# Kernel optimization log

Measured on AMD Instinct MI355X. Metric: run time of the kernel, lower is better.

## Reference

```python
import jax, jax.numpy as jnp
import numpy as np

BATCH = 8192
IN_F = 1024
OUT_F = 1024
GRID_SIZE = 5
SPLINE_ORDER = 3
GRID_LO, GRID_HI = -1.0, 1.0


def setup_inputs() -> dict:
    key = jax.random.key(0)
    k1, k2, k3, k4 = jax.random.split(key, 4)
    x = jax.random.normal(k1, (BATCH, IN_F), dtype=jnp.float32)
    # grid buffer: extended knot vector, same for every input feature
    h = (GRID_HI - GRID_LO) / GRID_SIZE
    knots = jnp.linspace(GRID_LO - SPLINE_ORDER * h, GRID_HI + SPLINE_ORDER * h,
                         GRID_SIZE + 2 * SPLINE_ORDER + 1, dtype=jnp.float32)
    grid = jnp.tile(knots[None, :], (IN_F, 1))  # [in, 12]
    fan_in_scale = 1.0 / np.sqrt(IN_F)
    base_weight = jax.random.normal(k2, (OUT_F, IN_F), dtype=jnp.float32) * fan_in_scale
    spline_weight = jax.random.normal(k3, (IN_F, GRID_SIZE + SPLINE_ORDER, OUT_F), dtype=jnp.float32) * 0.1
    spline_scaler = jax.random.normal(k4, (IN_F, OUT_F), dtype=jnp.float32) * fan_in_scale
    return {"x": x, "grid": grid, "base_weight": base_weight,
            "spline_weight": spline_weight, "spline_scaler": spline_scaler}


def b_splines(x, grid):
    """Cox-de Boor recursion. x: [B, in], grid: [in, G+2k+1] -> [B, in, G+k]."""
    xe = x[:, :, None]  # [B, in, 1]
    bases = ((xe >= grid[:, :-1]) & (xe < grid[:, 1:])).astype(x.dtype)  # [B, in, G+2k]
    for k in range(1, SPLINE_ORDER + 1):
        left = (xe - grid[:, :-(k + 1)]) / (grid[:, k:-1] - grid[:, :-(k + 1)])
        right = (grid[:, k + 1:] - xe) / (grid[:, k + 1:] - grid[:, 1:-k])
        bases = left * bases[:, :, :-1] + right * bases[:, :, 1:]
    return bases  # [B, in, G+k]


def reference(x, grid, base_weight, spline_weight, spline_scaler):
    # base branch: SiLU(x) @ W_base^T
    base_out = jax.nn.silu(x) @ base_weight.T  # [B, out]
    # spline branch
    basis = b_splines(x, grid)  # [B, in, G+k]
    scaled_w = spline_weight * spline_scaler[:, None, :]  # [in, G+k, out]
    spline_out = jnp.einsum('bik,iko->bo', basis, scaled_w)  # [B, out]
    return base_out + spline_out
```

## Files before the change

### kernel.cpp

```cpp
#include <hip/hip_runtime.h>
#include <cstdint>
#include <cstddef>

#define BATCH 8192
#define IN_F 1024
#define OUT_F 1024
#define NSPL 9
#define KDIM (IN_F * NSPL)

typedef __bf16 bf16x8 __attribute__((ext_vector_type(8)));
typedef float f32x4 __attribute__((ext_vector_type(4)));

__device__ __forceinline__ void g2l16(const void* g, void* l) {
  __builtin_amdgcn_global_load_lds(
      (__attribute__((address_space(1))) void*)(g),
      (__attribute__((address_space(3))) void*)(l),
      16, 0, 0);
}

__global__ void build_w(const float* __restrict__ bw, const float* __restrict__ sw,
                        const float* __restrict__ sc, __bf16* __restrict__ Wt) {
  __shared__ float s_sw[16 * 8 * 64];
  __shared__ float s_sc[16 * 64];
  __shared__ float s_bw[64 * 16];
  const int tid = threadIdx.x;
  const int o0 = (blockIdx.x & 15) * 64;
  const int i0 = (blockIdx.x >> 4) * 16;

#pragma unroll
  for (int it = 0; it < 32; ++it) {
    const int t = it * 256 + tid;
    const int i = t >> 9, r = (t >> 6) & 7, oo = t & 63;
    s_sw[t] = sw[((size_t)(i0 + i) * 8 + r) * OUT_F + o0 + oo];
  }
#pragma unroll
  for (int it = 0; it < 4; ++it) {
    const int t = it * 256 + tid;
    const int i = t >> 6, oo = t & 63;
    s_sc[t] = sc[(size_t)(i0 + i) * OUT_F + o0 + oo];
  }
#pragma unroll
  for (int it = 0; it < 4; ++it) {
    const int t = it * 256 + tid;
    const int oo = t >> 4, ii = t & 15;
    s_bw[t] = bw[(size_t)(o0 + oo) * IN_F + i0 + ii];
  }
  __syncthreads();

  const int oo = tid >> 2;
  const int isub = (tid & 3) * 4;
#pragma unroll
  for (int is = 0; is < 4; ++is) {
    const int i = isub + is;
    __bf16* dst = Wt + (size_t)(o0 + oo) * KDIM + (size_t)(i0 + i) * NSPL;
    dst[0] = (__bf16)s_bw[oo * 16 + i];
    const float scal = s_sc[i * 64 + oo];
#pragma unroll
    for (int r = 0; r < 8; ++r)
      dst[1 + r] = (__bf16)(s_sw[i * 512 + r * 64 + oo] * scal);
  }
}

__global__ void build_a(const float* __restrict__ x, __bf16* __restrict__ A) {
  __shared__ __align__(16) __bf16 rowbuf[KDIM];
  const int b = blockIdx.x;
  const int tid = threadIdx.x;
#pragma unroll
  for (int c = 0; c < IN_F / 256; ++c) {
    const int i = c * 256 + tid;
    const float v = x[(size_t)b * IN_F + i];
    float w[NSPL];
#pragma unroll
    for (int r = 0; r < NSPL; ++r) w[r] = 0.f;
    w[0] = v / (1.f + __expf(-v));
    const float p = (v + 2.2f) * 2.5f;
    const int cell = (int)floorf(p);
    if (cell >= 0 && cell <= 10 && v < 2.2f) {
      const float t = p - (float)cell;
      const float t2 = t * t, t3 = t2 * t;
      const float omt = 1.f - t;
      const float b0 = (1.f / 6.f) * omt * omt * omt;
      const float b1 = (1.f / 6.f) * (3.f * t3 - 6.f * t2 + 4.f);
      const float b2 = (1.f / 6.f) * (-3.f * t3 + 3.f * t2 + 3.f * t + 1.f);
      const float b3 = (1.f / 6.f) * t3;
      const int j0 = cell - 3;
      if (j0 + 0 >= 0 && j0 + 0 <= 7) w[1 + j0 + 0] = b0;
      if (j0 + 1 >= 0 && j0 + 1 <= 7) w[1 + j0 + 1] = b1;
      if (j0 + 2 >= 0 && j0 + 2 <= 7) w[1 + j0 + 2] = b2;
      if (j0 + 3 >= 0 && j0 + 3 <= 7) w[1 + j0 + 3] = b3;
    }
    __bf16* d = rowbuf + (size_t)i * NSPL;
#pragma unroll
    for (int r = 0; r < NSPL; ++r) d[r] = (__bf16)w[r];
  }
  __syncthreads();
  const uint4* src = (const uint4*)rowbuf;
  uint4* dst = (uint4*)(A + (size_t)b * KDIM);
  for (int t = tid; t < KDIM * 2 / 16; t += 256)
    dst[t] = src[t];
}

__global__ __launch_bounds__(256) void gemm_bt(const __bf16* __restrict__ A,
                                               const __bf16* __restrict__ W,
                                               float* __restrict__ out) {
  __shared__ __align__(16) __bf16 As[2 * 128 * 32];
  __shared__ __align__(16) __bf16 Bs[2 * 128 * 32];

  const int tid = threadIdx.x;
  const int wv = tid >> 6;
  const int lane = tid & 63;
  const int mb = blockIdx.x & 63;
  const int nb = blockIdx.x >> 6;
  const int m0 = mb * 128;
  const int n0 = nb * 128;
  const int wr = wv & 1;
  const int wc = wv >> 1;

  const int srow = lane >> 2;
  const int scol = (lane & 3) * 8;
  const __bf16* gA = A + (size_t)(m0 + wv * 32 + srow) * KDIM + scol;
  const __bf16* gB = W + (size_t)(n0 + wv * 32 + srow) * KDIM + scol;
  __bf16* lA = As + wv * 1024;
  __bf16* lB = Bs + wv * 1024;

  const int mrow = lane & 15;
  const int quad = lane >> 4;
  int aoff[4], boff[4];
#pragma unroll
  for (int mt = 0; mt < 4; ++mt) aoff[mt] = (wr * 64 + mt * 16 + mrow) * 32 + quad * 8;
#pragma unroll
  for (int nt = 0; nt < 4; ++nt) boff[nt] = (wc * 64 + nt * 16 + mrow) * 32 + quad * 8;

  f32x4 acc[4][4];
  const f32x4 zero = {0.f, 0.f, 0.f, 0.f};
#pragma unroll
  for (int mt = 0; mt < 4; ++mt)
#pragma unroll
    for (int nt = 0; nt < 4; ++nt) acc[mt][nt] = zero;

  for (int k0 = 0; k0 < KDIM; k0 += 64) {
    __syncthreads();
    g2l16(gA + k0, lA);
    g2l16(gA + k0 + (size_t)16 * KDIM, lA + 512);
    g2l16(gB + k0, lB);
    g2l16(gB + k0 + (size_t)16 * KDIM, lB + 512);
    g2l16(gA + k0 + 32, lA + 4096);
    g2l16(gA + k0 + 32 + (size_t)16 * KDIM, lA + 4096 + 512);
    g2l16(gB + k0 + 32, lB + 4096);
    g2l16(gB + k0 + 32 + (size_t)16 * KDIM, lB + 4096 + 512);
    __syncthreads();

    bf16x8 af[2][4], bfr[2][4];
#pragma unroll
    for (int h = 0; h < 2; ++h) {
#pragma unroll
      for (int mt = 0; mt < 4; ++mt) af[h][mt] = *(const bf16x8*)(As + h * 4096 + aoff[mt]);
#pragma unroll
      for (int nt = 0; nt < 4; ++nt) bfr[h][nt] = *(const bf16x8*)(Bs + h * 4096 + boff[nt]);
    }
#pragma unroll
    for (int h = 0; h < 2; ++h)
#pragma unroll
      for (int mt = 0; mt < 4; ++mt)
#pragma unroll
        for (int nt = 0; nt < 4; ++nt)
          acc[mt][nt] = __builtin_amdgcn_mfma_f32_16x16x32_bf16(af[h][mt], bfr[h][nt],
                                                                acc[mt][nt], 0, 0, 0);
  }

#pragma unroll
  for (int mt = 0; mt < 4; ++mt) {
#pragma unroll
    for (int nt = 0; nt < 4; ++nt) {
      const int col = n0 + wc * 64 + nt * 16 + mrow;
      const int rbase = m0 + wr * 64 + mt * 16 + quad * 4;
#pragma unroll
      for (int r = 0; r < 4; ++r)
        out[(size_t)(rbase + r) * OUT_F + col] = acc[mt][nt][r];
    }
  }
}

extern "C" void kernel_launch(void* const* d_in, const int* in_sizes, int n_in,
                              void* d_out, int out_size, void* d_ws, size_t ws_size,
                              hipStream_t stream) {
  const float* x  = (const float*)d_in[0];
  const float* bw = (const float*)d_in[2];
  const float* sw = (const float*)d_in[3];
  const float* sc = (const float*)d_in[4];
  float* out = (float*)d_out;

  __bf16* Wt = (__bf16*)d_ws;
  __bf16* Ab = (__bf16*)((char*)d_ws +
                         (size_t)OUT_F * KDIM * sizeof(__bf16));

  build_w<<<1024, 256, 0, stream>>>(bw, sw, sc, Wt);
  build_a<<<BATCH, 256, 0, stream>>>(x, Ab);
  gemm_bt<<<(BATCH / 128) * (OUT_F / 128), 256, 0, stream>>>(Ab, Wt, out);
}
```

Before: 315.2 us.

## Rebuild GEMM with 256x128 tiles, triple-buffered LDS pipeline and XOR swizzle

The bf16 GEMM moves to 512-thread blocks with 256x128 output tiles. It uses a three-stage LDS ring filled through global_load_lds, with vmcnt waits and raw barriers, so the loads for tile t+2 overlap the MFMAs for tile t. LDS columns are XOR-swizzled to reduce bank conflicts, block IDs are remapped for L2 locality, and s_setprio raises priority around the MFMA bursts. This is meant to hide global-load latency and remove the two full syncthreads per k-step, at the cost of more LDS (144KB), which may limit occupancy.

```diff
diff --git a/kernel.cpp b/kernel.cpp
--- a/kernel.cpp
+++ b/kernel.cpp
@@ -8,6 +8,11 @@
 #define NSPL 9
 #define KDIM (IN_F * NSPL)
 
+#define BM 256
+#define BN 128
+#define BK 64
+#define NTILE (KDIM / BK)
+
 typedef __bf16 bf16x8 __attribute__((ext_vector_type(8)));
 typedef float f32x4 __attribute__((ext_vector_type(4)));
 
@@ -16,6 +21,12 @@
       (__attribute__((address_space(1))) void*)(g),
       (__attribute__((address_space(3))) void*)(l),
       16, 0, 0);
+}
+
+__device__ __forceinline__ void barrier_raw() {
+  asm volatile("" ::: "memory");
+  __builtin_amdgcn_s_barrier();
+  asm volatile("" ::: "memory");
 }
 
 __global__ void build_w(const float* __restrict__ bw, const float* __restrict__ sw,
@@ -100,36 +111,53 @@
     dst[t] = src[t];
 }
 
-__global__ __launch_bounds__(256) void gemm_bt(const __bf16* __restrict__ A,
-                                               const __bf16* __restrict__ W,
-                                               float* __restrict__ out) {
-  __shared__ __align__(16) __bf16 As[2 * 128 * 32];
-  __shared__ __align__(16) __bf16 Bs[2 * 128 * 32];
+__global__ __launch_bounds__(512, 2) void gemm_bt(const __bf16* __restrict__ A,
+                                                  const __bf16* __restrict__ W,
+                                                  float* __restrict__ out) {
+  __shared__ __align__(16) __bf16 As[3][BM * BK];
+  __shared__ __align__(16) __bf16 Bs[3][BN * BK];
 
   const int tid = threadIdx.x;
   const int wv = tid >> 6;
   const int lane = tid & 63;
-  const int mb = blockIdx.x & 63;
-  const int nb = blockIdx.x >> 6;
-  const int m0 = mb * 128;
-  const int n0 = nb * 128;
-  const int wr = wv & 1;
-  const int wc = wv >> 1;
-
-  const int srow = lane >> 2;
-  const int scol = (lane & 3) * 8;
-  const __bf16* gA = A + (size_t)(m0 + wv * 32 + srow) * KDIM + scol;
-  const __bf16* gB = W + (size_t)(n0 + wv * 32 + srow) * KDIM + scol;
-  __bf16* lA = As + wv * 1024;
-  __bf16* lB = Bs + wv * 1024;
+
+  const int bid = blockIdx.x;
+  const int swz = (bid & 7) * 32 + (bid >> 3);
+  const int m0 = (swz & 31) * BM;
+  const int n0 = (swz >> 5) * BN;
+
+  const int wr = wv >> 1;
+  const int wc = wv & 1;
+
+  const int srow = lane >> 3;
+  const int usrc = (lane & 7) ^ srow;
+  const __bf16* gA = A + (size_t)(m0 + wv * 32 + srow) * KDIM + usrc * 8;
+  const __bf16* gB = W + (size_t)(n0 + wv * 16 + srow) * KDIM + usrc * 8;
+
+#define STAGE3_FIRST(q, tt)                                          \
+  do {                                                               \
+    const size_t ko = (size_t)(tt) * BK;                             \
+    g2l16(gA + ko,                      &As[q][(wv * 32 + 0) * BK]); \
+    g2l16(gA + ko + 8 * (size_t)KDIM,   &As[q][(wv * 32 + 8) * BK]); \
+    g2l16(gB + ko,                      &Bs[q][(wv * 16 + 0) * BK]); \
+  } while (0)
+#define STAGE3_SECOND(q, tt)                                          \
+  do {                                                                \
+    const size_t ko = (size_t)(tt) * BK;                              \
+    g2l16(gA + ko + 16 * (size_t)KDIM, &As[q][(wv * 32 + 16) * BK]);  \
+    g2l16(gA + ko + 24 * (size_t)KDIM, &As[q][(wv * 32 + 24) * BK]);  \
+    g2l16(gB + ko + 8 * (size_t)KDIM,  &Bs[q][(wv * 16 + 8) * BK]);   \
+  } while (0)
 
   const int mrow = lane & 15;
   const int quad = lane >> 4;
   int aoff[4], boff[4];
 #pragma unroll
-  for (int mt = 0; mt < 4; ++mt) aoff[mt] = (wr * 64 + mt * 16 + mrow) * 32 + quad * 8;
-#pragma unroll
-  for (int nt = 0; nt < 4; ++nt) boff[nt] = (wc * 64 + nt * 16 + mrow) * 32 + quad * 8;
+  for (int mt = 0; mt < 4; ++mt) aoff[mt] = (wr * 64 + mt * 16 + mrow) * BK;
+#pragma unroll
+  for (int nt = 0; nt < 4; ++nt) boff[nt] = (wc * 64 + nt * 16 + mrow) * BK;
+  const int colx0 = ((quad) ^ (mrow & 7)) * 8;
+  const int colx1 = ((4 + quad) ^ (mrow & 7)) * 8;
 
   f32x4 acc[4][4];
   const f32x4 zero = {0.f, 0.f, 0.f, 0.f};
@@ -138,34 +166,57 @@
 #pragma unroll
     for (int nt = 0; nt < 4; ++nt) acc[mt][nt] = zero;
 
-  for (int k0 = 0; k0 < KDIM; k0 += 64) {
-    __syncthreads();
-    g2l16(gA + k0, lA);
-    g2l16(gA + k0 + (size_t)16 * KDIM, lA + 512);
-    g2l16(gB + k0, lB);
-    g2l16(gB + k0 + (size_t)16 * KDIM, lB + 512);
-    g2l16(gA + k0 + 32, lA + 4096);
-    g2l16(gA + k0 + 32 + (size_t)16 * KDIM, lA + 4096 + 512);
-    g2l16(gB + k0 + 32, lB + 4096);
-    g2l16(gB + k0 + 32 + (size_t)16 * KDIM, lB + 4096 + 512);
-    __syncthreads();
-
-    bf16x8 af[2][4], bfr[2][4];
-#pragma unroll
-    for (int h = 0; h < 2; ++h) {
-#pragma unroll
-      for (int mt = 0; mt < 4; ++mt) af[h][mt] = *(const bf16x8*)(As + h * 4096 + aoff[mt]);
-#pragma unroll
-      for (int nt = 0; nt < 4; ++nt) bfr[h][nt] = *(const bf16x8*)(Bs + h * 4096 + boff[nt]);
+  STAGE3_FIRST(0, 0);
+  STAGE3_SECOND(0, 0);
+  STAGE3_FIRST(1, 1);
+  STAGE3_SECOND(1, 1);
+  asm volatile("s_waitcnt vmcnt(6)" ::: "memory");
+  barrier_raw();
+
+  int q = 0;
+  for (int t = 0; t < NTILE; ++t) {
+    const int qp = (q == 0) ? 2 : q - 1;
+
+    bf16x8 a0[4], b0[4];
+#pragma unroll
+    for (int mt = 0; mt < 4; ++mt) a0[mt] = *(const bf16x8*)(&As[q][aoff[mt] + colx0]);
+#pragma unroll
+    for (int nt = 0; nt < 4; ++nt) b0[nt] = *(const bf16x8*)(&Bs[q][boff[nt] + colx0]);
+    if (t + 2 < NTILE) STAGE3_FIRST(qp, t + 2);
+    barrier_raw();
+    __builtin_amdgcn_s_setprio(1);
+#pragma unroll
+    for (int mt = 0; mt < 4; ++mt)
+#pragma unroll
+      for (int nt = 0; nt < 4; ++nt)
+        acc[mt][nt] = __builtin_amdgcn_mfma_f32_16x16x32_bf16(a0[mt], b0[nt],
+                                                              acc[mt][nt], 0, 0, 0);
+    __builtin_amdgcn_s_setprio(0);
+    barrier_raw();
+
+    bf16x8 a1[4], b1[4];
+#pragma unroll
+    for (int mt = 0; mt < 4; ++mt) a1[mt] = *(const bf16x8*)(&As[q][aoff[mt] + colx1]);
+#pragma unroll
+    for (int nt = 0; nt < 4; ++nt) b1[nt] = *(const bf16x8*)(&Bs[q][boff[nt] + colx1]);
+    if (t + 2 < NTILE) {
+      STAGE3_SECOND(qp, t + 2);
+      asm volatile("s_waitcnt vmcnt(6)" ::: "memory");
+    } else {
+      asm volatile("s_waitcnt vmcnt(0)" ::: "memory");
     }
-#pragma unroll
-    for (int h = 0; h < 2; ++h)
-#pragma unroll
-      for (int mt = 0; mt < 4; ++mt)
-#pragma unroll
-        for (int nt = 0; nt < 4; ++nt)
-          acc[mt][nt] = __builtin_amdgcn_mfma_f32_16x16x32_bf16(af[h][mt], bfr[h][nt],
-                                                                acc[mt][nt], 0, 0, 0);
+    barrier_raw();
+    __builtin_amdgcn_s_setprio(1);
+#pragma unroll
+    for (int mt = 0; mt < 4; ++mt)
+#pragma unroll
+      for (int nt = 0; nt < 4; ++nt)
+        acc[mt][nt] = __builtin_amdgcn_mfma_f32_16x16x32_bf16(a1[mt], b1[nt],
+                                                              acc[mt][nt], 0, 0, 0);
+    __builtin_amdgcn_s_setprio(0);
+    barrier_raw();
+
+    q = (q == 2) ? 0 : q + 1;
   }
 
 #pragma unroll
@@ -179,6 +230,8 @@
         out[(size_t)(rbase + r) * OUT_F + col] = acc[mt][nt][r];
     }
   }
+#undef STAGE3_FIRST
+#undef STAGE3_SECOND
 }
 
 extern "C" void kernel_launch(void* const* d_in, const int* in_sizes, int n_in,
@@ -196,5 +249,5 @@
 
   build_w<<<1024, 256, 0, stream>>>(bw, sw, sc, Wt);
   build_a<<<BATCH, 256, 0, stream>>>(x, Ab);
-  gemm_bt<<<(BATCH / 128) * (OUT_F / 128), 256, 0, stream>>>(Ab, Wt, out);
-}
+  gemm_bt<<<(BATCH / BM) * (OUT_F / BN), 512, 0, stream>>>(Ab, Wt, out);
+}
```

Measured after the change: 319.3 us. Within noise of the previous version (+1.3%).
